# Performance work log

Measured on AMD Instinct MI355X. Metric: run time of the kernel, lower is better.

## Reference

```python
import jax, jax.numpy as jnp
import numpy as np

B, T, D, H = 4, 2048, 512, 8
DK = D // H
SCALE = 1.0 / np.sqrt(DK)
LN_EPS = 1e-6
NORM_EPS = 1e-8


def setup_inputs() -> dict:
    key = jax.random.key(0)
    ks = jax.random.split(key, 4)
    x = jax.random.normal(ks[0], (B, T, D), dtype=jnp.float32)
    mask = jax.random.randint(ks[1], (B, T), 0, 2) > 0  # True = invalid (padding)
    gain = 1.0 / np.sqrt(2)
    # xavier_uniform with gain for qkv_proj [3D, D] and out_proj [D, D]
    lim_qkv = gain * np.sqrt(6.0 / (3 * D + D))
    lim_out = gain * np.sqrt(6.0 / (D + D))
    qkv_w = jax.random.uniform(ks[2], (3 * D, D), jnp.float32, -lim_qkv, lim_qkv)
    out_w = jax.random.uniform(ks[3], (D, D), jnp.float32, -lim_out, lim_out)
    return {
        "x": x,
        "mask": mask,
        "ln_g": jnp.ones((D,), jnp.float32),
        "ln_b": jnp.zeros((D,), jnp.float32),
        "qkv_w": qkv_w,
        "qkv_b": jnp.zeros((3 * D,), jnp.float32),
        "out_w": out_w,
        "out_b": jnp.zeros((D,), jnp.float32),
    }


def _l2norm(v):
    # torch F.normalize: v / max(||v||_2, eps)
    n = jnp.sqrt(jnp.sum(v * v, axis=-1, keepdims=True))
    return v / jnp.maximum(n, NORM_EPS)


def reference(x, mask, ln_g, ln_b, qkv_w, qkv_b, out_w, out_b):
    # LayerNorm over last dim
    mu = jnp.mean(x, axis=-1, keepdims=True)
    var = jnp.mean((x - mu) ** 2, axis=-1, keepdims=True)
    xn = (x - mu) * jax.lax.rsqrt(var + LN_EPS) * ln_g + ln_b
    # fused QKV projection
    qkv = xn @ qkv_w.T + qkv_b                      # [B, T, 3D]
    qkv = qkv.reshape(B, T, 3, H, DK).transpose(2, 0, 3, 1, 4)  # [3, B, H, T, dk]
    Q, K, V = qkv[0], qkv[1], qkv[2]
    Q = _l2norm(Q)
    K = _l2norm(K)
    # explicit masked-softmax fallback path (mask provided)
    scores = jnp.einsum('bhtd,bhsd->bhts', Q, K) * SCALE
    scores = jnp.clip(scores, -10.0, 10.0)
    scores = jnp.where(mask[:, None, None, :], -10000.0, scores)
    attn = jax.nn.softmax(scores, axis=-1)          # (max-subtract is internal)
    attn_out = jnp.einsum('bhts,bhsd->bhtd', attn, V)  # [B, H, T, dk]
    attn_out = attn_out.transpose(0, 2, 1, 3).reshape(B, T, D)
    out = attn_out @ out_w.T + out_b
    return out * 0.5
```

## Files before the change

kernel.cpp:

```cpp
#include <hip/hip_runtime.h>


#define B_  4
#define T_  2048
#define D_  512
#define H_  8
#define DK_ 64
#define BT_ (B_*T_)

typedef unsigned short u16;
typedef unsigned char u8;
typedef u16 u16x8 __attribute__((ext_vector_type(8)));
typedef u16 u16x4 __attribute__((ext_vector_type(4)));
typedef __bf16 bf16x8 __attribute__((ext_vector_type(8)));
typedef float f32x4 __attribute__((ext_vector_type(4)));

__device__ inline u16 f2bf(float f) {
  return __builtin_bit_cast(u16, (__bf16)f);
}
__device__ inline float bf2f(u16 v) {
  return __builtin_bit_cast(float, (unsigned)v << 16);
}
__device__ inline f32x4 mfma16(u16x8 a, u16x8 b, f32x4 c) {
  return __builtin_amdgcn_mfma_f32_16x16x32_bf16(
      __builtin_bit_cast(bf16x8, a), __builtin_bit_cast(bf16x8, b), c, 0, 0, 0);
}

__global__ __launch_bounds__(256) void k_mask(const unsigned* __restrict__ mw,
                                              const u8* __restrict__ mb,
                                              int* __restrict__ out,
                                              u16* __restrict__ vones) {
  __shared__ unsigned sb[2];
  int tid = threadIdx.x;
  if (tid == 0) { sb[0] = 0; sb[1] = 0; }
  __syncthreads();
  unsigned big = 0, odd = 0;
  for (int i = tid; i < 2048; i += 256) {
    unsigned v = mw[i];
    big |= (v > 1u) ? 1u : 0u;
    if (i & 1) odd |= (v != 0u) ? 1u : 0u;
  }
  if (big) atomicOr(&sb[0], 1u);
  if (odd) atomicOr(&sb[1], 1u);
  __syncthreads();
  int fl = sb[0] ? 1 : (sb[1] ? 0 : 2);
  int i = blockIdx.x * 256 + tid;
  unsigned v = (fl == 1) ? (unsigned)mb[i] : (fl == 2) ? mw[2 * i] : mw[i];
  int m = (v != 0u) ? 1 : 0;
  out[i] = m;
  int b = i >> 11, t = i & (T_ - 1);
  int tl = t & 31;
  int gp, jp;
  if (tl < 16) { gp = tl >> 2; jp = tl & 3; }
  else { int u = tl - 16; gp = u >> 2; jp = 4 + (u & 3); }
  vones[((b * (T_ / 32) + (t >> 5)) * 4 + gp) * 8 + jp] = m ? (u16)0 : (u16)0x3F80;
}

__global__ __launch_bounds__(256) void k_cvt(const float* __restrict__ s1,
                                             u16* __restrict__ d1, int n1,
                                             const float* __restrict__ s2,
                                             u16* __restrict__ d2, int n2) {
  int i = (blockIdx.x * 256 + threadIdx.x) * 4;
  const float* s;
  u16* d;
  if (i < n1) {
    s = s1 + i; d = d1 + i;
  } else {
    int j = i - n1;
    if (j >= n2) return;
    s = s2 + j; d = d2 + j;
  }
  float4 v = *(const float4*)s;
  u16x4 o = {f2bf(v.x), f2bf(v.y), f2bf(v.z), f2bf(v.w)};
  *(u16x4*)d = o;
}

__global__ __launch_bounds__(256) void k_ln(const float* __restrict__ x,
                                            const float* __restrict__ gg,
                                            const float* __restrict__ bb,
                                            u16* __restrict__ xn) {
  int wave = threadIdx.x >> 6, lane = threadIdx.x & 63;
  size_t row = (size_t)blockIdx.x * 4 + wave;
  const float* xr = x + row * D_ + lane * 8;
  float v[8];
  *(float4*)(v)     = *(const float4*)(xr);
  *(float4*)(v + 4) = *(const float4*)(xr + 4);
  float s = 0.f;
#pragma unroll
  for (int i = 0; i < 8; i++) s += v[i];
#pragma unroll
  for (int o = 1; o < 64; o <<= 1) s += __shfl_xor(s, o);
  float mu = s * (1.0f / 512.0f);
  float vs = 0.f;
#pragma unroll
  for (int i = 0; i < 8; i++) { float t = v[i] - mu; vs += t * t; }
#pragma unroll
  for (int o = 1; o < 64; o <<= 1) vs += __shfl_xor(vs, o);
  float rs = rsqrtf(vs * (1.0f / 512.0f) + 1e-6f);
  float gv[8], bv[8];
  *(float4*)(gv)     = *(const float4*)(gg + lane * 8);
  *(float4*)(gv + 4) = *(const float4*)(gg + lane * 8 + 4);
  *(float4*)(bv)     = *(const float4*)(bb + lane * 8);
  *(float4*)(bv + 4) = *(const float4*)(bb + lane * 8 + 4);
  u16x8 o;
#pragma unroll
  for (int i = 0; i < 8; i++) o[i] = f2bf((v[i] - mu) * rs * gv[i] + bv[i]);
  *(u16x8*)(xn + row * D_ + lane * 8) = o;
}

template <int MODE>
__global__ __launch_bounds__(256) void k_gemm(const u16* __restrict__ A,
                                              const u16* __restrict__ Bt,
                                              const float* __restrict__ bias,
                                              float* __restrict__ Cf,
                                              u16* __restrict__ Qs,
                                              u16* __restrict__ Ks,
                                              u16* __restrict__ Vq,
                                              int M, int N, int K, float oscale) {
  __shared__ u16 lA[128 * 40];
  __shared__ u16 lB[128 * 40];
  int tid = threadIdx.x;
  int lane = tid & 63, w = tid >> 6;
  int g = lane >> 4, l15 = lane & 15;
  int wm = (w >> 1) * 64, wn = (w & 1) * 64;
  size_t m0 = (size_t)blockIdx.x * 128, n0 = (size_t)blockIdx.y * 128;
  f32x4 acc[4][4] = {};
  int arow = tid >> 2, acol = (tid & 3) * 8;
  const u16* Ab = A + (m0 + arow) * K + acol;
  const u16* Bb = Bt + (n0 + arow) * K + acol;
  size_t step64 = (size_t)64 * K;
  u16x8 a0 = *(const u16x8*)(Ab);
  u16x8 a1 = *(const u16x8*)(Ab + step64);
  u16x8 b0 = *(const u16x8*)(Bb);
  u16x8 b1 = *(const u16x8*)(Bb + step64);
  for (int k0 = 0; k0 < K; k0 += 32) {
    *(u16x8*)(lA + arow * 40 + acol) = a0;
    *(u16x8*)(lA + (arow + 64) * 40 + acol) = a1;
    *(u16x8*)(lB + arow * 40 + acol) = b0;
    *(u16x8*)(lB + (arow + 64) * 40 + acol) = b1;
    __syncthreads();
    if (k0 + 32 < K) {
      a0 = *(const u16x8*)(Ab + k0 + 32);
      a1 = *(const u16x8*)(Ab + step64 + k0 + 32);
      b0 = *(const u16x8*)(Bb + k0 + 32);
      b1 = *(const u16x8*)(Bb + step64 + k0 + 32);
    }
    u16x8 af[4], bf[4];
#pragma unroll
    for (int i = 0; i < 4; i++)
      af[i] = *(const u16x8*)(lA + (wm + i * 16 + l15) * 40 + g * 8);
#pragma unroll
    for (int i = 0; i < 4; i++)
      bf[i] = *(const u16x8*)(lB + (wn + i * 16 + l15) * 40 + g * 8);
#pragma unroll
    for (int i = 0; i < 4; i++)
#pragma unroll
      for (int j = 0; j < 4; j++) acc[i][j] = mfma16(af[i], bf[j], acc[i][j]);
    __syncthreads();
  }
  if constexpr (MODE == 0) {
#pragma unroll
    for (int i = 0; i < 4; i++) {
      size_t row = m0 + wm + i * 16 + g * 4;
#pragma unroll
      for (int j = 0; j < 4; j++) {
        size_t col = n0 + wn + j * 16 + l15;
        float bs = bias[col];
#pragma unroll
        for (int r = 0; r < 4; r++)
          Cf[(row + r) * (size_t)N + col] = (acc[i][j][r] + bs) * oscale;
      }
    }
  } else {
    int base_col = (int)n0 + wn;
    int proj = base_col >> 9;
    int hh = (base_col >> 6) & 7;
    u16* dbuf = (proj == 0) ? Qs : (proj == 1) ? Ks : Vq;
    float bs[4];
#pragma unroll
    for (int j = 0; j < 4; j++) bs[j] = bias[base_col + j * 16 + l15];
#pragma unroll
    for (int i = 0; i < 4; i++) {
      size_t row = m0 + wm + i * 16 + g * 4;
#pragma unroll
      for (int r = 0; r < 4; r++) {
        float v4[4];
        float s2 = 0.f;
#pragma unroll
        for (int j = 0; j < 4; j++) {
          float t = acc[i][j][r] + bs[j];
          v4[j] = t;
          s2 += t * t;
        }
        s2 += __shfl_xor(s2, 1);
        s2 += __shfl_xor(s2, 2);
        s2 += __shfl_xor(s2, 4);
        s2 += __shfl_xor(s2, 8);
        float nrm = fmaxf(sqrtf(s2), 1e-8f);
        float sc = (proj == 0) ? 0.18033688f / nrm
                 : (proj == 1) ? 1.0f / nrm : 1.0f;
        size_t rr = row + r;
        int bb_ = (int)(rr >> 11);
        int tt = (int)(rr & (T_ - 1));
        u16* dst = dbuf + ((size_t)(bb_ * H_ + hh) * T_ + tt) * 64;
#pragma unroll
        for (int j = 0; j < 4; j++) dst[j * 16 + l15] = f2bf(v4[j] * sc);
      }
    }
  }
}

__global__ __launch_bounds__(256) void k_vt(const u16* __restrict__ Vq,
                                            const int* __restrict__ m32,
                                            u16* __restrict__ Vf) {
  __shared__ u16 vt[64 * 66];
  int bh = blockIdx.x, t0 = blockIdx.y * 64;
  int b = bh >> 3;
  int u = threadIdx.x, tl = u >> 2, q = u & 3;
  const u16* src = Vq + ((size_t)bh * T_ + t0 + tl) * 64 + q * 16;
  u16x8 vr0 = *(const u16x8*)(src);
  u16x8 vr1 = *(const u16x8*)(src + 8);
  u16 keep = m32[b * T_ + t0 + tl] ? (u16)0 : (u16)0xFFFFu;
#pragma unroll
  for (int i = 0; i < 8; i++) { vr0[i] &= keep; vr1[i] &= keep; }
#pragma unroll
  for (int i = 0; i < 8; i++) {
    vt[(q * 16 + i) * 66 + tl] = vr0[i];
    vt[(q * 16 + 8 + i) * 66 + tl] = vr1[i];
  }
  __syncthreads();
  int d = u & 63, gg = u >> 6;
#pragma unroll
  for (int sb = 0; sb < 2; sb++) {
    u16x8 o;
#pragma unroll
    for (int j = 0; j < 8; j++) {
      int psi = (j < 4) ? (gg * 4 + j) : (16 + gg * 4 + (j - 4));
      o[j] = vt[d * 66 + sb * 32 + psi];
    }
    size_t sblk = (size_t)(t0 >> 5) + sb;
    *(u16x8*)(Vf + ((((size_t)bh * (T_ / 32) + sblk) * 4 + gg) * 64 + d) * 8) = o;
  }
}

__global__ __launch_bounds__(512) void k_attn(const u16* __restrict__ Qs,
                                              const u16* __restrict__ Ks,
                                              const u16* __restrict__ Vf,
                                              const u16* __restrict__ Vones,
                                              u16* __restrict__ AO) {
  int i = blockIdx.x;
  int bh = (i & 7) * 4 + ((i >> 3) >> 4);
  int t0 = ((i >> 3) & 15) * 128;
  int b = bh >> 3, h = bh & 7;
  int tid = threadIdx.x, w = tid >> 6, lane = tid & 63;
  int g = lane >> 4, l15 = lane & 15;
  const u16* Qp = Qs + ((size_t)bh * T_ + t0 + w * 16 + l15) * 64 + g * 8;
  u16x8 bq0 = *(const u16x8*)(Qp);
  u16x8 bq1 = *(const u16x8*)(Qp + 32);
  const u16* Kb = Ks + (size_t)bh * T_ * 64;
  const u16* Vb = Vf + ((((size_t)bh * (T_ / 32)) * 4 + g) * 64 + l15) * 8;
  const u16* Ob = Vones + (size_t)b * (T_ / 32) * 32 + g * 8;
  f32x4 acc[4] = {};
  f32x4 accd = {};
  for (int s0 = 0; s0 < T_; s0 += 64) {
    f32x4 sa[4];
#pragma unroll
    for (int nf = 0; nf < 4; nf++) {
      const u16* kp = Kb + (size_t)(s0 + nf * 16 + l15) * 64 + g * 8;
      u16x8 k0 = *(const u16x8*)(kp);
      u16x8 k1 = *(const u16x8*)(kp + 32);
      f32x4 z = {0.f, 0.f, 0.f, 0.f};
      z = mfma16(k0, bq0, z);
      z = mfma16(k1, bq1, z);
      sa[nf] = z;
    }
    u16 pb[4][4];
#pragma unroll
    for (int nf = 0; nf < 4; nf++)
#pragma unroll
      for (int r = 0; r < 4; r++) pb[nf][r] = f2bf(exp2f(sa[nf][r]));
    u16x8 pa0 = {pb[0][0], pb[0][1], pb[0][2], pb[0][3],
                 pb[1][0], pb[1][1], pb[1][2], pb[1][3]};
    u16x8 pa1 = {pb[2][0], pb[2][1], pb[2][2], pb[2][3],
                 pb[3][0], pb[3][1], pb[3][2], pb[3][3]};
    u16x8 of0 = {}, of1 = {};
    if (l15 == 0) {
      of0 = *(const u16x8*)(Ob + (s0 >> 5) * 32);
      of1 = *(const u16x8*)(Ob + (s0 >> 5) * 32 + 32);
    }
    accd = mfma16(pa0, of0, accd);
    accd = mfma16(pa1, of1, accd);
    const u16* vs0 = Vb + (size_t)(s0 >> 5) * (4 * 64 * 8);
#pragma unroll
    for (int nd = 0; nd < 4; nd++) {
      u16x8 vf0 = *(const u16x8*)(vs0 + (size_t)nd * 16 * 8);
      u16x8 vf1 = *(const u16x8*)(vs0 + (size_t)(4 * 64 + nd * 16) * 8);
      acc[nd] = mfma16(pa0, vf0, acc[nd]);
      acc[nd] = mfma16(pa1, vf1, acc[nd]);
    }
  }
  float inv[4];
#pragma unroll
  for (int r = 0; r < 4; r++) inv[r] = 1.0f / __shfl(accd[r], g * 16);
#pragma unroll
  for (int r = 0; r < 4; r++) {
    size_t trow = (size_t)b * T_ + t0 + w * 16 + g * 4 + r;
#pragma unroll
    for (int nd = 0; nd < 4; nd++) {
      AO[trow * D_ + h * 64 + nd * 16 + l15] = f2bf(acc[nd][r] * inv[r]);
    }
  }
}

extern "C" void kernel_launch(void* const* d_in, const int* in_sizes, int n_in,
                              void* d_out, int out_size, void* d_ws, size_t ws_size,
                              hipStream_t stream) {
  (void)in_sizes; (void)n_in; (void)out_size; (void)ws_size;
  const float* x     = (const float*)d_in[0];
  const void*  maskp = d_in[1];
  const float* ln_g  = (const float*)d_in[2];
  const float* ln_b  = (const float*)d_in[3];
  const float* qkv_w = (const float*)d_in[4];
  const float* qkv_b = (const float*)d_in[5];
  const float* out_w = (const float*)d_in[6];
  const float* out_b = (const float*)d_in[7];

  char* ws = (char*)d_ws;
  size_t off = 0;
  auto alloc = [&](size_t bytes) -> void* {
    void* p = ws + off;
    off += (bytes + 255) & ~(size_t)255;
    return p;
  };
  u16*   xn   = (u16*)alloc((size_t)BT_ * D_ * 2);
  u16*   qw   = (u16*)alloc((size_t)3 * D_ * D_ * 2);
  u16*   ow   = (u16*)alloc((size_t)D_ * D_ * 2);
  u16*   Vq   = (u16*)alloc((size_t)B_ * H_ * T_ * DK_ * 2);
  u16*   Vf   = (u16*)alloc((size_t)B_ * H_ * T_ * DK_ * 2);
  int*   m32  = (int*)alloc((size_t)BT_ * 4);
  u16*   von  = (u16*)alloc((size_t)B_ * (T_ / 32) * 32 * 2);
  u16*   Qs   = (u16*)d_out;
  u16*   Ks   = Qs + (size_t)B_ * H_ * T_ * DK_;
  u16*   ao   = xn;

  k_mask<<<dim3(BT_ / 256), dim3(256), 0, stream>>>(
      (const unsigned*)maskp, (const u8*)maskp, m32, von);
  k_cvt<<<dim3(D_ * D_ / 256), dim3(256), 0, stream>>>(
      qkv_w, qw, 3 * D_ * D_, out_w, ow, D_ * D_);
  k_ln<<<dim3(BT_ / 4), dim3(256), 0, stream>>>(x, ln_g, ln_b, xn);
  k_gemm<1><<<dim3(BT_ / 128, 3 * D_ / 128), dim3(256), 0, stream>>>(
      xn, qw, qkv_b, nullptr, Qs, Ks, Vq, BT_, 3 * D_, D_, 1.0f);
  k_vt<<<dim3(B_ * H_, T_ / 64), dim3(256), 0, stream>>>(Vq, m32, Vf);
  k_attn<<<dim3(B_ * H_ * T_ / 128), dim3(512), 0, stream>>>(Qs, Ks, Vf, von, ao);
  k_gemm<0><<<dim3(BT_ / 128, D_ / 128), dim3(256), 0, stream>>>(
      ao, ow, out_b, (float*)d_out, nullptr, nullptr, nullptr, BT_, D_, D_, 0.5f);
}
```

Measured before the change: 282.7 us.

## Split attention key dimension in two and combine partials in a new kernel

The attention kernel now splits the key/value range into two halves, doubling the grid from 512 to 1024 blocks. Each block writes unnormalized bf16 partial accumulators and fp32 denominators to workspace, and a new combine kernel sums the halves, normalizes, and writes the head-interleaved output. This is meant to raise CU occupancy on a GPU with many CUs, since 512 blocks underfill it. In exchange it adds an extra launch, extra global traffic, and a bf16 rounding of the partials. The partial buffer reuses the Vq buffer space.

```diff
diff --git a/kernel.cpp b/kernel.cpp
--- a/kernel.cpp
+++ b/kernel.cpp
@@ -7,6 +7,7 @@
 #define H_  8
 #define DK_ 64
 #define BT_ (B_*T_)
+#define BHT_ (B_*H_*T_)
 
 typedef unsigned short u16;
 typedef unsigned char u8;
@@ -243,15 +244,18 @@
   }
 }
 
-__global__ __launch_bounds__(512) void k_attn(const u16* __restrict__ Qs,
-                                              const u16* __restrict__ Ks,
-                                              const u16* __restrict__ Vf,
-                                              const u16* __restrict__ Vones,
-                                              u16* __restrict__ AO) {
+__global__ __launch_bounds__(512, 8) void k_attn(const u16* __restrict__ Qs,
+                                                 const u16* __restrict__ Ks,
+                                                 const u16* __restrict__ Vf,
+                                                 const u16* __restrict__ Vones,
+                                                 u16* __restrict__ accP,
+                                                 float* __restrict__ denP) {
   int i = blockIdx.x;
-  int bh = (i & 7) * 4 + ((i >> 3) >> 4);
-  int t0 = ((i >> 3) & 15) * 128;
-  int b = bh >> 3, h = bh & 7;
+  int rest = i >> 3;
+  int bh = (i & 7) * 4 + (rest >> 5);
+  int t0 = ((rest >> 1) & 15) * 128;
+  int sp = rest & 1;
+  int b = bh >> 3;
   int tid = threadIdx.x, w = tid >> 6, lane = tid & 63;
   int g = lane >> 4, l15 = lane & 15;
   const u16* Qp = Qs + ((size_t)bh * T_ + t0 + w * 16 + l15) * 64 + g * 8;
@@ -262,7 +266,8 @@
   const u16* Ob = Vones + (size_t)b * (T_ / 32) * 32 + g * 8;
   f32x4 acc[4] = {};
   f32x4 accd = {};
-  for (int s0 = 0; s0 < T_; s0 += 64) {
+  int s_begin = sp * (T_ / 2);
+  for (int s0 = s_begin; s0 < s_begin + T_ / 2; s0 += 64) {
     f32x4 sa[4];
 #pragma unroll
     for (int nf = 0; nf < 4; nf++) {
@@ -299,17 +304,37 @@
       acc[nd] = mfma16(pa1, vf1, acc[nd]);
     }
   }
-  float inv[4];
-#pragma unroll
-  for (int r = 0; r < 4; r++) inv[r] = 1.0f / __shfl(accd[r], g * 16);
+  u16* ap = accP + (size_t)sp * ((size_t)BHT_ * 64);
 #pragma unroll
   for (int r = 0; r < 4; r++) {
-    size_t trow = (size_t)b * T_ + t0 + w * 16 + g * 4 + r;
-#pragma unroll
-    for (int nd = 0; nd < 4; nd++) {
-      AO[trow * D_ + h * 64 + nd * 16 + l15] = f2bf(acc[nd][r] * inv[r]);
-    }
-  }
+    size_t rowid = (size_t)bh * T_ + t0 + w * 16 + g * 4 + r;
+#pragma unroll
+    for (int nd = 0; nd < 4; nd++)
+      ap[rowid * 64 + nd * 16 + l15] = f2bf(acc[nd][r]);
+  }
+  if (l15 == 0) {
+    float* dp = denP + (size_t)sp * BHT_;
+#pragma unroll
+    for (int r = 0; r < 4; r++)
+      dp[(size_t)bh * T_ + t0 + w * 16 + g * 4 + r] = accd[r];
+  }
+}
+
+__global__ __launch_bounds__(256) void k_comb(const u16* __restrict__ accP,
+                                              const float* __restrict__ denP,
+                                              u16* __restrict__ AO) {
+  int idx = blockIdx.x * 256 + threadIdx.x;
+  int row = idx >> 4;
+  int d4 = (idx & 15) * 4;
+  u16x4 a0 = *(const u16x4*)(accP + (size_t)row * 64 + d4);
+  u16x4 a1 = *(const u16x4*)(accP + (size_t)BHT_ * 64 + (size_t)row * 64 + d4);
+  float inv = 1.0f / (denP[row] + denP[BHT_ + row]);
+  int bh = row >> 11, t = row & (T_ - 1);
+  int b = bh >> 3, h = bh & 7;
+  u16x4 o;
+#pragma unroll
+  for (int e = 0; e < 4; e++) o[e] = f2bf((bf2f(a0[e]) + bf2f(a1[e])) * inv);
+  *(u16x4*)(AO + ((size_t)b * T_ + t) * D_ + h * 64 + d4) = o;
 }
 
 extern "C" void kernel_launch(void* const* d_in, const int* in_sizes, int n_in,
@@ -335,8 +360,11 @@
   u16*   xn   = (u16*)alloc((size_t)BT_ * D_ * 2);
   u16*   qw   = (u16*)alloc((size_t)3 * D_ * D_ * 2);
   u16*   ow   = (u16*)alloc((size_t)D_ * D_ * 2);
+  u16*   Vf   = (u16*)alloc((size_t)B_ * H_ * T_ * DK_ * 2);
   u16*   Vq   = (u16*)alloc((size_t)B_ * H_ * T_ * DK_ * 2);
-  u16*   Vf   = (u16*)alloc((size_t)B_ * H_ * T_ * DK_ * 2);
+  u16*   accP = Vq;
+  alloc((size_t)2 * BHT_ * 64 * 2 - (size_t)B_ * H_ * T_ * DK_ * 2);
+  float* denP = (float*)alloc((size_t)2 * BHT_ * 4);
   int*   m32  = (int*)alloc((size_t)BT_ * 4);
   u16*   von  = (u16*)alloc((size_t)B_ * (T_ / 32) * 32 * 2);
   u16*   Qs   = (u16*)d_out;
@@ -351,7 +379,9 @@
   k_gemm<1><<<dim3(BT_ / 128, 3 * D_ / 128), dim3(256), 0, stream>>>(
       xn, qw, qkv_b, nullptr, Qs, Ks, Vq, BT_, 3 * D_, D_, 1.0f);
   k_vt<<<dim3(B_ * H_, T_ / 64), dim3(256), 0, stream>>>(Vq, m32, Vf);
-  k_attn<<<dim3(B_ * H_ * T_ / 128), dim3(512), 0, stream>>>(Qs, Ks, Vf, von, ao);
+  k_attn<<<dim3(B_ * H_ * T_ / 128 * 2), dim3(512), 0, stream>>>(
+      Qs, Ks, Vf, von, accP, denP);
+  k_comb<<<dim3(BHT_ * 16 / 256), dim3(256), 0, stream>>>(accP, denP, ao);
   k_gemm<0><<<dim3(BT_ / 128, D_ / 128), dim3(256), 0, stream>>>(
       ao, ow, out_b, (float*)d_out, nullptr, nullptr, nullptr, BT_, D_, D_, 0.5f);
 }
```

Result: slower. 324.6 us (+14.8%).
